# Optimization experiments

Measured on AMD Instinct MI355X. Metric: run time of the kernel, lower is better.

Reference implementation:

```python
import jax, jax.numpy as jnp
import numpy as np

N_NODES = 100000
N_EDGES = 1600000
IN_DIM = 128
HID = 128
OUT = 40


def setup_inputs() -> dict:
    key = jax.random.key(0)
    ks = jax.random.split(key, 8)
    x = jax.random.normal(ks[0], (N_NODES, IN_DIM), dtype=jnp.float32)
    edge_index = jax.random.randint(ks[1], (2, N_EDGES), 0, N_NODES, dtype=jnp.int64)
    def glorot(k, fan_in, fan_out):
        s = jnp.sqrt(6.0 / (fan_in + fan_out)).astype(jnp.float32)
        return jax.random.uniform(k, (fan_in, fan_out), jnp.float32, -s, s)
    return {
        "x": x,
        "edge_index": edge_index,
        "W1": glorot(ks[2], IN_DIM, HID), "b1": jnp.zeros((HID,), jnp.float32),
        "W2": glorot(ks[3], HID, HID),    "b2": jnp.zeros((HID,), jnp.float32),
        "W3": glorot(ks[4], HID, HID),    "b3": jnp.zeros((HID,), jnp.float32),
        "Wl": glorot(ks[5], HID, OUT),    "bl": jnp.zeros((OUT,), jnp.float32),
    }


def _gcn_norm(edge_index, num_nodes):
    # PyG GCNConv default: add self-loops, symmetric normalization.
    loops = jnp.arange(num_nodes, dtype=edge_index.dtype)
    src = jnp.concatenate([edge_index[0], loops])
    dst = jnp.concatenate([edge_index[1], loops])
    deg = jax.ops.segment_sum(jnp.ones_like(dst, dtype=jnp.float32), dst,
                              num_segments=num_nodes)
    dis = jnp.where(deg > 0, jax.lax.rsqrt(deg), 0.0)  # deg^{-1/2}
    norm = dis[src] * dis[dst]  # [E+N]
    return src, dst, norm


def _gcn_conv(x, W, b, src, dst, norm, num_nodes):
    h = x @ W                                   # [N, F_out]
    msg = h[src] * norm[:, None]                # gather + scale
    out = jax.ops.segment_sum(msg, dst, num_segments=num_nodes)
    return out + b


def reference(x, edge_index, W1, b1, W2, b2, W3, b3, Wl, bl):
    n = x.shape[0]
    src, dst, norm = _gcn_norm(edge_index, n)
    h = jax.nn.relu(_gcn_conv(x, W1, b1, src, dst, norm, n))
    h = jax.nn.relu(_gcn_conv(h, W2, b2, src, dst, norm, n))
    h = _gcn_conv(h, W3, b3, src, dst, norm, n)
    # dropout p=0.5 is identity in eval mode
    return h @ Wl + bl
```

## Files before the change

kernel.cpp:

```cpp
#include <hip/hip_runtime.h>

typedef __attribute__((ext_vector_type(8))) short sh8;
typedef __attribute__((ext_vector_type(4))) float f4;

__device__ __forceinline__ float bf2f(unsigned short u) {
    union { unsigned int u; float f; } c; c.u = ((unsigned int)u) << 16; return c.f;
}
__device__ __forceinline__ unsigned short f2bf(float f) {
    union { float f; unsigned int u; } c; c.f = f;
    unsigned int x = c.u;
    unsigned int r = (x + 0x7fffu + ((x >> 16) & 1u)) >> 16;
    return (unsigned short)r;
}
__device__ __forceinline__ void bfsplit(float x, short& hi, short& lo) {
    unsigned short h = f2bf(x);
    float r = x - bf2f(h);
    hi = (short)h;
    lo = (short)f2bf(r);
}

__global__ void k_zero_cnt(int* cnt, int N) {
    int i = blockIdx.x * 256 + threadIdx.x;
    if (i < N) cnt[i] = 0;
}

__global__ void k_count(const int* __restrict__ dst, int* __restrict__ cnt, int E, int N) {
    int E4 = E >> 2;
    for (int i = blockIdx.x * 256 + threadIdx.x; i < E4; i += gridDim.x * 256) {
        int4 d = ((const int4*)dst)[i];
        if ((unsigned)d.x < (unsigned)N) atomicAdd(&cnt[d.x], 1);
        if ((unsigned)d.y < (unsigned)N) atomicAdd(&cnt[d.y], 1);
        if ((unsigned)d.z < (unsigned)N) atomicAdd(&cnt[d.z], 1);
        if ((unsigned)d.w < (unsigned)N) atomicAdd(&cnt[d.w], 1);
    }
    if (blockIdx.x == 0) {
        for (int e = (E4 << 2) + threadIdx.x; e < E; e += 256) {
            int d = dst[e];
            if ((unsigned)d < (unsigned)N) atomicAdd(&cnt[d], 1);
        }
    }
}

#define SCAN_B 256
__global__ void k_scan_a(const int* __restrict__ cnt, int* __restrict__ rowptr,
                         int* __restrict__ bsum, float* __restrict__ dis, int N) {
    __shared__ int sh[SCAN_B];
    int t = threadIdx.x, i = blockIdx.x * SCAN_B + t;
    int v = (i < N) ? cnt[i] : 0;
    if (i < N) dis[i] = rsqrtf((float)(v + 1));
    sh[t] = v; __syncthreads();
    for (int off = 1; off < SCAN_B; off <<= 1) {
        int x = (t >= off) ? sh[t - off] : 0;
        __syncthreads();
        sh[t] += x;
        __syncthreads();
    }
    int incl = sh[t];
    if (i < N) rowptr[i] = incl - v;
    if (t == SCAN_B - 1) bsum[blockIdx.x] = incl;
}

__global__ void k_scan_b(int* bsum, int NB) {
    __shared__ int sh[512];
    int t = threadIdx.x;
    int v = (t < NB) ? bsum[t] : 0;
    sh[t] = v; __syncthreads();
    for (int off = 1; off < 512; off <<= 1) {
        int x = (t >= off) ? sh[t - off] : 0;
        __syncthreads();
        sh[t] += x;
        __syncthreads();
    }
    if (t < NB) bsum[t] = sh[t] - v;
}

__global__ void k_scan_c(int* __restrict__ rowptr, int* __restrict__ cursor,
                         const int* __restrict__ bsum, int N) {
    int i = blockIdx.x * 256 + threadIdx.x;
    if (i < N) {
        int r = rowptr[i] + bsum[blockIdx.x];
        rowptr[i] = r;
        cursor[i] = r;
    }
}

__global__ void k_fill(const int* __restrict__ src, const int* __restrict__ dst,
                       int* __restrict__ cursor, int* __restrict__ csrc, int E, int N) {
    int g = blockIdx.x & 7;
    int j = blockIdx.x >> 3;
    int nb = gridDim.x >> 3;
    int lo = (int)((long long)g * N / 8);
    int hi = (int)((long long)(g + 1) * N / 8);
    int E4 = E >> 2;
    for (int i = j * 256 + threadIdx.x; i < E4; i += nb * 256) {
        int4 d4 = ((const int4*)dst)[i];
        int e = i << 2;
        #pragma unroll
        for (int q = 0; q < 4; ++q) {
            int d = (q == 0) ? d4.x : (q == 1) ? d4.y : (q == 2) ? d4.z : d4.w;
            if (d < lo || d >= hi) continue;
            int s = src[e + q];
            if ((unsigned)s >= (unsigned)N) continue;
            int p = atomicAdd(&cursor[d], 1);
            csrc[p] = s;
        }
    }
    if (blockIdx.x == 0) {
        for (int e = (E4 << 2) + threadIdx.x; e < E; e += 256) {
            int d = dst[e];
            int s = src[e];
            if ((unsigned)d >= (unsigned)N || (unsigned)s >= (unsigned)N) continue;
            int p = atomicAdd(&cursor[d], 1);
            csrc[p] = s;
        }
    }
}

__global__ __launch_bounds__(256)
void k_gemm128_a32(const float* __restrict__ X,
                   const float* __restrict__ W,
                   unsigned short* __restrict__ H, int nPairs) {
    int wave = threadIdx.x >> 6;
    int lane = threadIdx.x & 63;
    int ln = lane & 15, quad = lane >> 4;
    int c0 = (wave & 1) * 64;
    int subTile = wave >> 1;

    sh8 bh[4][4], blo[4][4];
    #pragma unroll
    for (int nt = 0; nt < 4; ++nt) {
        int col = c0 + nt * 16 + ln;
        #pragma unroll
        for (int kt = 0; kt < 4; ++kt) {
            int k0 = kt * 32 + quad * 8;
            #pragma unroll
            for (int j = 0; j < 8; ++j) {
                short h, l;
                bfsplit(W[(k0 + j) * 128 + col], h, l);
                bh[nt][kt][j] = h; blo[nt][kt][j] = l;
            }
        }
    }

    for (int p = blockIdx.x; p < nPairs; p += gridDim.x) {
        int nodeBase = p * 32 + subTile * 16;
        const float* xrow = X + (nodeBase + ln) * 128 + quad * 8;
        sh8 ah[4], al[4];
        #pragma unroll
        for (int kt = 0; kt < 4; ++kt) {
            f4 v0 = *(const f4*)(xrow + kt * 32);
            f4 v1 = *(const f4*)(xrow + kt * 32 + 4);
            #pragma unroll
            for (int j = 0; j < 4; ++j) {
                short h, l;
                bfsplit(v0[j], h, l); ah[kt][j] = h; al[kt][j] = l;
                bfsplit(v1[j], h, l); ah[kt][j + 4] = h; al[kt][j + 4] = l;
            }
        }

        f4 acc[4] = { {0.f,0.f,0.f,0.f}, {0.f,0.f,0.f,0.f}, {0.f,0.f,0.f,0.f}, {0.f,0.f,0.f,0.f} };
        #pragma unroll
        for (int kt = 0; kt < 4; ++kt)
            #pragma unroll
            for (int nt = 0; nt < 4; ++nt) {
                acc[nt] = __builtin_amdgcn_mfma_f32_16x16x32_bf16(ah[kt], bh[nt][kt], acc[nt], 0, 0, 0);
                acc[nt] = __builtin_amdgcn_mfma_f32_16x16x32_bf16(ah[kt], blo[nt][kt], acc[nt], 0, 0, 0);
                acc[nt] = __builtin_amdgcn_mfma_f32_16x16x32_bf16(al[kt], bh[nt][kt], acc[nt], 0, 0, 0);
            }

        #pragma unroll
        for (int nt = 0; nt < 4; ++nt) {
            int col = c0 + nt * 16 + ln;
            #pragma unroll
            for (int r = 0; r < 4; ++r)
                H[(nodeBase + quad * 4 + r) * 128 + col] = f2bf(acc[nt][r]);
        }
    }
}

__global__ __launch_bounds__(256)
void k_gemm128_a16(const unsigned short* __restrict__ X,
                   const float* __restrict__ W,
                   unsigned short* __restrict__ H, int nPairs) {
    int wave = threadIdx.x >> 6;
    int lane = threadIdx.x & 63;
    int ln = lane & 15, quad = lane >> 4;
    int c0 = (wave & 1) * 64;
    int subTile = wave >> 1;

    sh8 bh[4][4], blo[4][4];
    #pragma unroll
    for (int nt = 0; nt < 4; ++nt) {
        int col = c0 + nt * 16 + ln;
        #pragma unroll
        for (int kt = 0; kt < 4; ++kt) {
            int k0 = kt * 32 + quad * 8;
            #pragma unroll
            for (int j = 0; j < 8; ++j) {
                short h, l;
                bfsplit(W[(k0 + j) * 128 + col], h, l);
                bh[nt][kt][j] = h; blo[nt][kt][j] = l;
            }
        }
    }

    for (int p = blockIdx.x; p < nPairs; p += gridDim.x) {
        int nodeBase = p * 32 + subTile * 16;
        const unsigned short* xrow = X + (nodeBase + ln) * 128 + quad * 8;
        sh8 a[4];
        #pragma unroll
        for (int kt = 0; kt < 4; ++kt) a[kt] = *(const sh8*)(xrow + kt * 32);

        f4 acc[4] = { {0.f,0.f,0.f,0.f}, {0.f,0.f,0.f,0.f}, {0.f,0.f,0.f,0.f}, {0.f,0.f,0.f,0.f} };
        #pragma unroll
        for (int kt = 0; kt < 4; ++kt)
            #pragma unroll
            for (int nt = 0; nt < 4; ++nt) {
                acc[nt] = __builtin_amdgcn_mfma_f32_16x16x32_bf16(a[kt], bh[nt][kt], acc[nt], 0, 0, 0);
                acc[nt] = __builtin_amdgcn_mfma_f32_16x16x32_bf16(a[kt], blo[nt][kt], acc[nt], 0, 0, 0);
            }

        #pragma unroll
        for (int nt = 0; nt < 4; ++nt) {
            int col = c0 + nt * 16 + ln;
            #pragma unroll
            for (int r = 0; r < 4; ++r)
                H[(nodeBase + quad * 4 + r) * 128 + col] = f2bf(acc[nt][r]);
        }
    }
}

__global__ __launch_bounds__(256)
void k_agg(const unsigned short* __restrict__ H,
           unsigned short* __restrict__ O,
           const float* __restrict__ dis,
           const int* __restrict__ rowptr,
           const int* __restrict__ cnt,
           const int* __restrict__ csrc,
           const float* __restrict__ bias,
           int relu, int N) {
    int n = (blockIdx.x * 256 + threadIdx.x) >> 5;
    int sub = threadIdx.x & 31;
    if (n >= N) return;

    float dn = dis[n];
    float a0, a1, a2, a3;
    {
        uint2 v = *(const uint2*)(H + (size_t)n * 128 + sub * 4);
        float w = dn * dn;
        a0 = w * bf2f((unsigned short)v.x);
        a1 = w * bf2f((unsigned short)(v.x >> 16));
        a2 = w * bf2f((unsigned short)v.y);
        a3 = w * bf2f((unsigned short)(v.y >> 16));
    }

    int start = rowptr[n];
    int e = cnt[n];
    int i = 0;
    for (; i + 8 <= e; i += 8) {
        int s[8];
        #pragma unroll
        for (int q = 0; q < 8; ++q) s[q] = csrc[start + i + q];
        uint2 v[8];
        #pragma unroll
        for (int q = 0; q < 8; ++q) v[q] = *(const uint2*)(H + (size_t)s[q] * 128 + sub * 4);
        float w[8];
        #pragma unroll
        for (int q = 0; q < 8; ++q) w[q] = dis[s[q]] * dn;
        #pragma unroll
        for (int q = 0; q < 8; ++q) {
            a0 += w[q] * bf2f((unsigned short)v[q].x);
            a1 += w[q] * bf2f((unsigned short)(v[q].x >> 16));
            a2 += w[q] * bf2f((unsigned short)v[q].y);
            a3 += w[q] * bf2f((unsigned short)(v[q].y >> 16));
        }
    }
    if (i + 4 <= e) {
        int s[4];
        #pragma unroll
        for (int q = 0; q < 4; ++q) s[q] = csrc[start + i + q];
        uint2 v[4];
        #pragma unroll
        for (int q = 0; q < 4; ++q) v[q] = *(const uint2*)(H + (size_t)s[q] * 128 + sub * 4);
        #pragma unroll
        for (int q = 0; q < 4; ++q) {
            float w = dis[s[q]] * dn;
            a0 += w * bf2f((unsigned short)v[q].x);
            a1 += w * bf2f((unsigned short)(v[q].x >> 16));
            a2 += w * bf2f((unsigned short)v[q].y);
            a3 += w * bf2f((unsigned short)(v[q].y >> 16));
        }
        i += 4;
    }
    for (; i < e; ++i) {
        int s0 = csrc[start + i];
        uint2 v = *(const uint2*)(H + (size_t)s0 * 128 + sub * 4);
        float w = dis[s0] * dn;
        a0 += w * bf2f((unsigned short)v.x);
        a1 += w * bf2f((unsigned short)(v.x >> 16));
        a2 += w * bf2f((unsigned short)v.y);
        a3 += w * bf2f((unsigned short)(v.y >> 16));
    }

    f4 b = *(const f4*)(bias + sub * 4);
    a0 += b[0]; a1 += b[1]; a2 += b[2]; a3 += b[3];
    if (relu) {
        a0 = fmaxf(a0, 0.f); a1 = fmaxf(a1, 0.f);
        a2 = fmaxf(a2, 0.f); a3 = fmaxf(a3, 0.f);
    }
    uint2 ov;
    ov.x = (unsigned int)f2bf(a0) | ((unsigned int)f2bf(a1) << 16);
    ov.y = (unsigned int)f2bf(a2) | ((unsigned int)f2bf(a3) << 16);
    *(uint2*)(O + (size_t)n * 128 + sub * 4) = ov;
}

__global__ __launch_bounds__(256)
void k_gemm_final(const unsigned short* __restrict__ X,
                  const float* __restrict__ W,
                  const float* __restrict__ bl,
                  float* __restrict__ OUT, int nTiles) {
    int wave = threadIdx.x >> 6;
    int lane = threadIdx.x & 63;
    int ln = lane & 15, quad = lane >> 4;
    int tile = blockIdx.x * 4 + wave;
    if (tile >= nTiles) return;

    sh8 bh[3][4], blo[3][4];
    #pragma unroll
    for (int nt = 0; nt < 3; ++nt) {
        int col = nt * 16 + ln;
        bool valid = (col < 40);
        #pragma unroll
        for (int kt = 0; kt < 4; ++kt) {
            int k0 = kt * 32 + quad * 8;
            #pragma unroll
            for (int j = 0; j < 8; ++j) {
                short h = 0, l = 0;
                if (valid) bfsplit(W[(k0 + j) * 40 + col], h, l);
                bh[nt][kt][j] = h; blo[nt][kt][j] = l;
            }
        }
    }

    int nodeBase = tile * 16;
    const unsigned short* xrow = X + (nodeBase + ln) * 128 + quad * 8;
    sh8 a[4];
    #pragma unroll
    for (int kt = 0; kt < 4; ++kt) a[kt] = *(const sh8*)(xrow + kt * 32);

    f4 acc[3] = { {0.f,0.f,0.f,0.f}, {0.f,0.f,0.f,0.f}, {0.f,0.f,0.f,0.f} };
    #pragma unroll
    for (int kt = 0; kt < 4; ++kt)
        #pragma unroll
        for (int nt = 0; nt < 3; ++nt) {
            acc[nt] = __builtin_amdgcn_mfma_f32_16x16x32_bf16(a[kt], bh[nt][kt], acc[nt], 0, 0, 0);
            acc[nt] = __builtin_amdgcn_mfma_f32_16x16x32_bf16(a[kt], blo[nt][kt], acc[nt], 0, 0, 0);
        }

    #pragma unroll
    for (int nt = 0; nt < 3; ++nt) {
        int col = nt * 16 + ln;
        if (col < 40) {
            float bv = bl[col];
            #pragma unroll
            for (int r = 0; r < 4; ++r)
                OUT[(nodeBase + quad * 4 + r) * 40 + col] = acc[nt][r] + bv;
        }
    }
}

extern "C" void kernel_launch(void* const* d_in, const int* in_sizes, int n_in,
                              void* d_out, int out_size, void* d_ws, size_t ws_size,
                              hipStream_t stream) {
    const float* x  = (const float*)d_in[0];
    const int*   ei = (const int*)d_in[1];
    const float* W1 = (const float*)d_in[2];
    const float* b1 = (const float*)d_in[3];
    const float* W2 = (const float*)d_in[4];
    const float* b2 = (const float*)d_in[5];
    const float* W3 = (const float*)d_in[6];
    const float* b3 = (const float*)d_in[7];
    const float* Wl = (const float*)d_in[8];
    const float* bl = (const float*)d_in[9];

    const int N = in_sizes[0] / 128;
    const int E = in_sizes[1] / 2;
    const int* srcIdx = ei;
    const int* dstIdx = ei + E;

    char* ws = (char*)d_ws;
    size_t off = 0;
    auto alloc = [&](size_t bytes) { void* p = ws + off; off += (bytes + 511) & ~(size_t)511; return p; };
    int*   cnt     = (int*)  alloc((size_t)N * 4);
    int*   rowptr  = (int*)  alloc((size_t)N * 4);
    int*   cursor  = (int*)  alloc((size_t)N * 4);
    float* dis     = (float*)alloc((size_t)N * 4);
    int*   bsum    = (int*)  alloc(512 * 4);
    int*   csrc    = (int*)  alloc((size_t)E * 4);
    unsigned short* h0 = (unsigned short*)alloc((size_t)N * 128 * 2);
    unsigned short* h1 = (unsigned short*)alloc((size_t)N * 128 * 2);

    const int gN = (N + 255) / 256;
    const int nPairs = N / 32;
    const int nTiles = N / 16;
    const int gAgg = (N * 32 + 255) / 256;
    const int gPart = 1024;

    k_zero_cnt<<<gN, 256, 0, stream>>>(cnt, N);
    k_count<<<768, 256, 0, stream>>>(dstIdx, cnt, E, N);
    k_scan_a<<<gN, 256, 0, stream>>>(cnt, rowptr, bsum, dis, N);
    k_scan_b<<<1, 512, 0, stream>>>(bsum, gN);
    k_scan_c<<<gN, 256, 0, stream>>>(rowptr, cursor, bsum, N);
    k_fill<<<gPart, 256, 0, stream>>>(srcIdx, dstIdx, cursor, csrc, E, N);

    k_gemm128_a32<<<768, 256, 0, stream>>>(x, W1, h0, nPairs);
    k_agg<<<gAgg, 256, 0, stream>>>(h0, h1, dis, rowptr, cnt, csrc, b1, 1, N);
    k_gemm128_a16<<<768, 256, 0, stream>>>(h1, W2, h0, nPairs);
    k_agg<<<gAgg, 256, 0, stream>>>(h0, h1, dis, rowptr, cnt, csrc, b2, 1, N);
    k_gemm128_a16<<<768, 256, 0, stream>>>(h1, W3, h0, nPairs);
    k_agg<<<gAgg, 256, 0, stream>>>(h0, h1, dis, rowptr, cnt, csrc, b3, 0, N);
    k_gemm_final<<<(nTiles + 3) / 4, 256, 0, stream>>>(h1, Wl, bl, (float*)d_out, nTiles);
}
```

Measured before the change: 541.1 us.

## Prescale GEMM output by source degree norm and split aggregation across half-warps

The GEMM epilogues now multiply each output row by dis[node], so the aggregation kernel no longer gathers dis[src] per edge and applies dis[dst] once at the end. The aggregation kernel is restructured: each 32-lane group splits into two halves that process alternating edges with 16-byte loads of 8 features per lane, then combines the halves with a shuffle. The count and fill launches also get larger grids. The intent is fewer scattered loads and wider memory transactions in the gather. In exchange, rounding happens after prescaling in bf16, and half the lanes sit idle during the epilogue.

```diff
diff --git a/kernel.cpp b/kernel.cpp
--- a/kernel.cpp
+++ b/kernel.cpp
@@ -119,6 +119,7 @@
 __global__ __launch_bounds__(256)
 void k_gemm128_a32(const float* __restrict__ X,
                    const float* __restrict__ W,
+                   const float* __restrict__ dis,
                    unsigned short* __restrict__ H, int nPairs) {
     int wave = threadIdx.x >> 6;
     int lane = threadIdx.x & 63;
@@ -168,12 +169,15 @@
                 acc[nt] = __builtin_amdgcn_mfma_f32_16x16x32_bf16(al[kt], bh[nt][kt], acc[nt], 0, 0, 0);
             }
 
+        float ds[4];
+        #pragma unroll
+        for (int r = 0; r < 4; ++r) ds[r] = dis[nodeBase + quad * 4 + r];
         #pragma unroll
         for (int nt = 0; nt < 4; ++nt) {
             int col = c0 + nt * 16 + ln;
             #pragma unroll
             for (int r = 0; r < 4; ++r)
-                H[(nodeBase + quad * 4 + r) * 128 + col] = f2bf(acc[nt][r]);
+                H[(nodeBase + quad * 4 + r) * 128 + col] = f2bf(acc[nt][r] * ds[r]);
         }
     }
 }
@@ -181,6 +185,7 @@
 __global__ __launch_bounds__(256)
 void k_gemm128_a16(const unsigned short* __restrict__ X,
                    const float* __restrict__ W,
+                   const float* __restrict__ dis,
                    unsigned short* __restrict__ H, int nPairs) {
     int wave = threadIdx.x >> 6;
     int lane = threadIdx.x & 63;
@@ -220,12 +225,15 @@
                 acc[nt] = __builtin_amdgcn_mfma_f32_16x16x32_bf16(a[kt], blo[nt][kt], acc[nt], 0, 0, 0);
             }
 
+        float ds[4];
+        #pragma unroll
+        for (int r = 0; r < 4; ++r) ds[r] = dis[nodeBase + quad * 4 + r];
         #pragma unroll
         for (int nt = 0; nt < 4; ++nt) {
             int col = c0 + nt * 16 + ln;
             #pragma unroll
             for (int r = 0; r < 4; ++r)
-                H[(nodeBase + quad * 4 + r) * 128 + col] = f2bf(acc[nt][r]);
+                H[(nodeBase + quad * 4 + r) * 128 + col] = f2bf(acc[nt][r] * ds[r]);
         }
     }
 }
@@ -240,78 +248,72 @@
            const float* __restrict__ bias,
            int relu, int N) {
     int n = (blockIdx.x * 256 + threadIdx.x) >> 5;
-    int sub = threadIdx.x & 31;
     if (n >= N) return;
-
-    float dn = dis[n];
-    float a0, a1, a2, a3;
-    {
-        uint2 v = *(const uint2*)(H + (size_t)n * 128 + sub * 4);
-        float w = dn * dn;
-        a0 = w * bf2f((unsigned short)v.x);
-        a1 = w * bf2f((unsigned short)(v.x >> 16));
-        a2 = w * bf2f((unsigned short)v.y);
-        a3 = w * bf2f((unsigned short)(v.y >> 16));
-    }
+    int lane = threadIdx.x & 31;
+    int sub  = lane & 15;
+    int half = lane >> 4;
+
+    float a0 = 0.f, a1 = 0.f, a2 = 0.f, a3 = 0.f;
+    float a4 = 0.f, a5 = 0.f, a6 = 0.f, a7 = 0.f;
+
+    auto addrow = [&](uint4 v) {
+        a0 += bf2f((unsigned short)v.x);
+        a1 += bf2f((unsigned short)(v.x >> 16));
+        a2 += bf2f((unsigned short)v.y);
+        a3 += bf2f((unsigned short)(v.y >> 16));
+        a4 += bf2f((unsigned short)v.z);
+        a5 += bf2f((unsigned short)(v.z >> 16));
+        a6 += bf2f((unsigned short)v.w);
+        a7 += bf2f((unsigned short)(v.w >> 16));
+    };
+
+    if (half == 0)
+        addrow(*(const uint4*)(H + (size_t)n * 128 + sub * 8));
 
     int start = rowptr[n];
     int e = cnt[n];
     int i = 0;
     for (; i + 8 <= e; i += 8) {
-        int s[8];
-        #pragma unroll
-        for (int q = 0; q < 8; ++q) s[q] = csrc[start + i + q];
-        uint2 v[8];
-        #pragma unroll
-        for (int q = 0; q < 8; ++q) v[q] = *(const uint2*)(H + (size_t)s[q] * 128 + sub * 4);
-        float w[8];
-        #pragma unroll
-        for (int q = 0; q < 8; ++q) w[q] = dis[s[q]] * dn;
-        #pragma unroll
-        for (int q = 0; q < 8; ++q) {
-            a0 += w[q] * bf2f((unsigned short)v[q].x);
-            a1 += w[q] * bf2f((unsigned short)(v[q].x >> 16));
-            a2 += w[q] * bf2f((unsigned short)v[q].y);
-            a3 += w[q] * bf2f((unsigned short)(v[q].y >> 16));
-        }
-    }
-    if (i + 4 <= e) {
         int s[4];
         #pragma unroll
-        for (int q = 0; q < 4; ++q) s[q] = csrc[start + i + q];
-        uint2 v[4];
-        #pragma unroll
-        for (int q = 0; q < 4; ++q) v[q] = *(const uint2*)(H + (size_t)s[q] * 128 + sub * 4);
-        #pragma unroll
-        for (int q = 0; q < 4; ++q) {
-            float w = dis[s[q]] * dn;
-            a0 += w * bf2f((unsigned short)v[q].x);
-            a1 += w * bf2f((unsigned short)(v[q].x >> 16));
-            a2 += w * bf2f((unsigned short)v[q].y);
-            a3 += w * bf2f((unsigned short)(v[q].y >> 16));
-        }
-        i += 4;
-    }
-    for (; i < e; ++i) {
-        int s0 = csrc[start + i];
-        uint2 v = *(const uint2*)(H + (size_t)s0 * 128 + sub * 4);
-        float w = dis[s0] * dn;
-        a0 += w * bf2f((unsigned short)v.x);
-        a1 += w * bf2f((unsigned short)(v.x >> 16));
-        a2 += w * bf2f((unsigned short)v.y);
-        a3 += w * bf2f((unsigned short)(v.y >> 16));
-    }
-
-    f4 b = *(const f4*)(bias + sub * 4);
-    a0 += b[0]; a1 += b[1]; a2 += b[2]; a3 += b[3];
-    if (relu) {
-        a0 = fmaxf(a0, 0.f); a1 = fmaxf(a1, 0.f);
-        a2 = fmaxf(a2, 0.f); a3 = fmaxf(a3, 0.f);
-    }
-    uint2 ov;
-    ov.x = (unsigned int)f2bf(a0) | ((unsigned int)f2bf(a1) << 16);
-    ov.y = (unsigned int)f2bf(a2) | ((unsigned int)f2bf(a3) << 16);
-    *(uint2*)(O + (size_t)n * 128 + sub * 4) = ov;
+        for (int q = 0; q < 4; ++q) s[q] = csrc[start + i + 2 * q + half];
+        uint4 v[4];
+        #pragma unroll
+        for (int q = 0; q < 4; ++q) v[q] = *(const uint4*)(H + (size_t)s[q] * 128 + sub * 8);
+        #pragma unroll
+        for (int q = 0; q < 4; ++q) addrow(v[q]);
+    }
+    for (int j = i + half; j < e; j += 2) {
+        int s = csrc[start + j];
+        addrow(*(const uint4*)(H + (size_t)s * 128 + sub * 8));
+    }
+
+    a0 += __shfl_xor(a0, 16); a1 += __shfl_xor(a1, 16);
+    a2 += __shfl_xor(a2, 16); a3 += __shfl_xor(a3, 16);
+    a4 += __shfl_xor(a4, 16); a5 += __shfl_xor(a5, 16);
+    a6 += __shfl_xor(a6, 16); a7 += __shfl_xor(a7, 16);
+
+    if (half == 0) {
+        float dn = dis[n];
+        f4 b0 = *(const f4*)(bias + sub * 8);
+        f4 b1 = *(const f4*)(bias + sub * 8 + 4);
+        a0 = a0 * dn + b0[0]; a1 = a1 * dn + b0[1];
+        a2 = a2 * dn + b0[2]; a3 = a3 * dn + b0[3];
+        a4 = a4 * dn + b1[0]; a5 = a5 * dn + b1[1];
+        a6 = a6 * dn + b1[2]; a7 = a7 * dn + b1[3];
+        if (relu) {
+            a0 = fmaxf(a0, 0.f); a1 = fmaxf(a1, 0.f);
+            a2 = fmaxf(a2, 0.f); a3 = fmaxf(a3, 0.f);
+            a4 = fmaxf(a4, 0.f); a5 = fmaxf(a5, 0.f);
+            a6 = fmaxf(a6, 0.f); a7 = fmaxf(a7, 0.f);
+        }
+        uint4 ov;
+        ov.x = (unsigned int)f2bf(a0) | ((unsigned int)f2bf(a1) << 16);
+        ov.y = (unsigned int)f2bf(a2) | ((unsigned int)f2bf(a3) << 16);
+        ov.z = (unsigned int)f2bf(a4) | ((unsigned int)f2bf(a5) << 16);
+        ov.w = (unsigned int)f2bf(a6) | ((unsigned int)f2bf(a7) << 16);
+        *(uint4*)(O + (size_t)n * 128 + sub * 8) = ov;
+    }
 }
 
 __global__ __launch_bounds__(256)
@@ -404,20 +406,20 @@
     const int nPairs = N / 32;
     const int nTiles = N / 16;
     const int gAgg = (N * 32 + 255) / 256;
-    const int gPart = 1024;
+    const int gPart = 2048;
 
     k_zero_cnt<<<gN, 256, 0, stream>>>(cnt, N);
-    k_count<<<768, 256, 0, stream>>>(dstIdx, cnt, E, N);
+    k_count<<<1568, 256, 0, stream>>>(dstIdx, cnt, E, N);
     k_scan_a<<<gN, 256, 0, stream>>>(cnt, rowptr, bsum, dis, N);
     k_scan_b<<<1, 512, 0, stream>>>(bsum, gN);
     k_scan_c<<<gN, 256, 0, stream>>>(rowptr, cursor, bsum, N);
     k_fill<<<gPart, 256, 0, stream>>>(srcIdx, dstIdx, cursor, csrc, E, N);
 
-    k_gemm128_a32<<<768, 256, 0, stream>>>(x, W1, h0, nPairs);
+    k_gemm128_a32<<<768, 256, 0, stream>>>(x, W1, dis, h0, nPairs);
     k_agg<<<gAgg, 256, 0, stream>>>(h0, h1, dis, rowptr, cnt, csrc, b1, 1, N);
-    k_gemm128_a16<<<768, 256, 0, stream>>>(h1, W2, h0, nPairs);
+    k_gemm128_a16<<<768, 256, 0, stream>>>(h1, W2, dis, h0, nPairs);
     k_agg<<<gAgg, 256, 0, stream>>>(h0, h1, dis, rowptr, cnt, csrc, b2, 1, N);
-    k_gemm128_a16<<<768, 256, 0, stream>>>(h1, W3, h0, nPairs);
+    k_gemm128_a16<<<768, 256, 0, stream>>>(h1, W3, dis, h0, nPairs);
     k_agg<<<gAgg, 256, 0, stream>>>(h0, h1, dis, rowptr, cnt, csrc, b3, 0, N);
     k_gemm_final<<<(nTiles + 3) / 4, 256, 0, stream>>>(h1, Wl, bl, (float*)d_out, nTiles);
 }
```

Result: no change. 539.1 us (-0.4%).
